# Kernel optimization log

Hardware: AMD Instinct MI355X
Metric: run time of the kernel (lower is better)

The kernel has to match this reference:

```python
import jax, jax.numpy as jnp
import numpy as np

N = 8192
E = 262144
H = 8
D_IN = 256
D_OUT = 256
D_PRIME = D_OUT // H  # is_concat=True


def setup_inputs() -> dict:
    key = jax.random.key(0)
    k_x, k_e, k_ww, k_wb, k_aw, k_ab = jax.random.split(key, 6)
    scale_w = 1.0 / np.sqrt(D_IN)
    scale_a = 1.0 / np.sqrt(2 * D_PRIME)
    return {
        "x": jax.random.normal(k_x, (N, D_IN), dtype=jnp.float32),
        "edge_index": jax.random.randint(k_e, (2, E), 0, N, dtype=jnp.int64),
        "W_w": jax.random.uniform(k_ww, (H, D_PRIME, D_IN), jnp.float32, -scale_w, scale_w),
        "W_b": jax.random.uniform(k_wb, (H, D_PRIME), jnp.float32, -scale_w, scale_w),
        "a_w": jax.random.uniform(k_aw, (H, 1, 2 * D_PRIME), jnp.float32, -scale_a, scale_a),
        "a_b": jax.random.uniform(k_ab, (H, 1), jnp.float32, -scale_a, scale_a),
    }


def reference(x, edge_index, W_w, W_b, a_w, a_b):
    n = x.shape[0]
    vi, vj = edge_index[0], edge_index[1]
    heads = []
    for k in range(W_w.shape[0]):  # small fixed head loop
        Wx = x @ W_w[k].T + W_b[k]                       # [N, d']
        pair = jnp.concatenate([Wx[vi], Wx[vj]], axis=-1)  # [E, 2d']
        e = jax.nn.leaky_relu(pair @ a_w[k].T + a_b[k], negative_slope=0.2)[:, 0]  # [E]
        # dense NxN score matrix: non-edges keep score 0 and DO participate in softmax,
        # duplicate edges accumulate -- matches torch scatter_add_ + Softmax(dim=-1)
        A = jnp.zeros((n, n), dtype=x.dtype).at[vi, vj].add(e)
        heads.append(jax.nn.softmax(A, axis=-1) @ Wx)     # [N, d']
    xp = jnp.stack(heads)                                 # [H, N, d']
    xp = jnp.transpose(xp, (1, 0, 2)).reshape(n, -1)      # is_concat=True
    return jax.nn.elu(xp)
```

## Files before the change

### kernel.cpp

```cpp
#include <hip/hip_runtime.h>


constexpr int N_NODES = 8192;
constexpr int E_EDGES = 262144;
constexpr int DIN = 256;
constexpr int DOUT = 256;
constexpr int MAXROW = 96;

__device__ __forceinline__ float leaky02(float v) { return v > 0.f ? v : 0.2f * v; }

__global__ __launch_bounds__(256) void gemm_fused(
    const float* __restrict__ x, const float* __restrict__ W,
    const float* __restrict__ Wb, const float* __restrict__ a_w,
    float* __restrict__ Wx, float* __restrict__ asrc_t,
    float* __restrict__ adst_t, float* __restrict__ colsum)
{
    __shared__ float As[16][68];
    __shared__ float Bs[16][68];
    __shared__ float redS[2][64];
    __shared__ float redD[2][64];
    __shared__ float csum[64];
    const int t = threadIdx.x;
    const int r0 = blockIdx.x * 64;
    const int c0 = blockIdx.y * 64;
    const int lr = t & 15, lc = t >> 4;
    const int sr = t >> 2, sk = (t & 3) * 4;

    if (t < 64) { redS[0][t] = 0.f; redS[1][t] = 0.f; redD[0][t] = 0.f; redD[1][t] = 0.f; csum[t] = 0.f; }

    float acc[4][4] = {};
    for (int kc = 0; kc < DIN; kc += 16) {
        float4 av = *(const float4*)&x[(size_t)(r0 + sr) * DIN + kc + sk];
        float4 bv = *(const float4*)&W[(size_t)(c0 + sr) * DIN + kc + sk];
        __syncthreads();
        As[sk + 0][sr] = av.x; As[sk + 1][sr] = av.y;
        As[sk + 2][sr] = av.z; As[sk + 3][sr] = av.w;
        Bs[sk + 0][sr] = bv.x; Bs[sk + 1][sr] = bv.y;
        Bs[sk + 2][sr] = bv.z; Bs[sk + 3][sr] = bv.w;
        __syncthreads();
#pragma unroll
        for (int k = 0; k < 16; ++k) {
            float4 a = *(const float4*)&As[k][lr * 4];
            float4 b = *(const float4*)&Bs[k][lc * 4];
            acc[0][0] += a.x * b.x; acc[0][1] += a.x * b.y; acc[0][2] += a.x * b.z; acc[0][3] += a.x * b.w;
            acc[1][0] += a.y * b.x; acc[1][1] += a.y * b.y; acc[1][2] += a.y * b.z; acc[1][3] += a.y * b.w;
            acc[2][0] += a.z * b.x; acc[2][1] += a.z * b.y; acc[2][2] += a.z * b.z; acc[2][3] += a.z * b.w;
            acc[3][0] += a.w * b.x; acc[3][1] += a.w * b.y; acc[3][2] += a.w * b.z; acc[3][3] += a.w * b.w;
        }
    }
    const int ccol = c0 + lc * 4;
    float4 bias = *(const float4*)&Wb[ccol];
#pragma unroll
    for (int i = 0; i < 4; ++i) {
        acc[i][0] += bias.x; acc[i][1] += bias.y; acc[i][2] += bias.z; acc[i][3] += bias.w;
        float4 o; o.x = acc[i][0]; o.y = acc[i][1]; o.z = acc[i][2]; o.w = acc[i][3];
        *(float4*)&Wx[(size_t)(r0 + lr * 4 + i) * DOUT + ccol] = o;
    }

    const int hloc = lc >> 3;
    const int hgl = blockIdx.y * 2 + hloc;
    const int dbase = (lc & 7) * 4;
    float aws[4], awd[4];
#pragma unroll
    for (int j = 0; j < 4; ++j) {
        aws[j] = a_w[hgl * 64 + dbase + j];
        awd[j] = a_w[hgl * 64 + 32 + dbase + j];
    }
#pragma unroll
    for (int i = 0; i < 4; ++i) {
        float ps = acc[i][0] * aws[0] + acc[i][1] * aws[1] + acc[i][2] * aws[2] + acc[i][3] * aws[3];
        float pd = acc[i][0] * awd[0] + acc[i][1] * awd[1] + acc[i][2] * awd[2] + acc[i][3] * awd[3];
        atomicAdd(&redS[hloc][lr * 4 + i], ps);
        atomicAdd(&redD[hloc][lr * 4 + i], pd);
    }
#pragma unroll
    for (int j = 0; j < 4; ++j)
        atomicAdd(&csum[lc * 4 + j], acc[0][j] + acc[1][j] + acc[2][j] + acc[3][j]);
    __syncthreads();
    if (t < 128) {
        int hh = t >> 6, r = t & 63;
        asrc_t[(size_t)(r0 + r) * 8 + blockIdx.y * 2 + hh] = redS[hh][r];
    } else {
        int u = t - 128; int hh = u >> 6, r = u & 63;
        adst_t[(size_t)(r0 + r) * 8 + blockIdx.y * 2 + hh] = redD[hh][r];
    }
    if (t < 64) atomicAdd(&colsum[c0 + t], csum[t]);
}

__global__ __launch_bounds__(256) void bucket_kernel(const int* __restrict__ eidx,
                                                     int* __restrict__ counts,
                                                     int* __restrict__ colbuf) {
    int e = blockIdx.x * 256 + threadIdx.x;
    int vi = eidx[e];
    int vj = eidx[E_EDGES + e];
    int c = atomicAdd(&counts[vi], 1);
    if (c < MAXROW) colbuf[(size_t)vi * MAXROW + c] = vj;
}

__global__ __launch_bounds__(256) void row_softmax(
    const int* __restrict__ counts, const int* __restrict__ colbuf,
    const float* __restrict__ Wx, const float* __restrict__ asrc_t,
    const float* __restrict__ adst_t, const float* __restrict__ a_b,
    const float* __restrict__ colsum, float* __restrict__ out)
{
    const int w = threadIdx.x >> 6;
    const int lane = threadIdx.x & 63;
    const int i = blockIdx.x * 4 + w;

    __shared__ alignas(16) int   colsL[4][MAXROW];
    __shared__ alignas(16) float wv[4][MAXROW][8];
    __shared__ alignas(16) float sv[4][MAXROW];

    int len = counts[i];
    if (len > MAXROW) len = MAXROW;

    for (int p = lane; p < len; p += 64) colsL[w][p] = colbuf[(size_t)i * MAXROW + p];
    __builtin_amdgcn_wave_barrier();

    const float4 as0 = *(const float4*)&asrc_t[(size_t)i * 8];
    const float4 as1 = *(const float4*)&asrc_t[(size_t)i * 8 + 4];
    const float4 ab0 = *(const float4*)&a_b[0];
    const float4 ab1 = *(const float4*)&a_b[4];
    float sab[8] = {as0.x + ab0.x, as0.y + ab0.y, as0.z + ab0.z, as0.w + ab0.w,
                    as1.x + ab1.x, as1.y + ab1.y, as1.z + ab1.z, as1.w + ab1.w};

    float base[8];

    if (len <= 64) {
        const bool act = lane < len;
        const int c = act ? colsL[w][lane] : 0;
        const int c_cmp = act ? c : (0x40000000 + lane);
        bool dupb = false;
        for (int k = 1; k < 64; ++k) {
            int cq = __shfl(c_cmp, (lane - k) & 63);
            dupb = dupb || ((k <= lane) && (cq == c_cmp));
        }
        const bool isrep = act && !dupb;
        const int nd = __popcll(__ballot(isrep));
        const bool anydup = (nd != len);

        const float4 ad0 = *(const float4*)&adst_t[(size_t)c * 8];
        const float4 ad1 = *(const float4*)&adst_t[(size_t)c * 8 + 4];
        float s[8], sm[8];
        s[0] = leaky02(sab[0] + ad0.x); s[1] = leaky02(sab[1] + ad0.y);
        s[2] = leaky02(sab[2] + ad0.z); s[3] = leaky02(sab[3] + ad0.w);
        s[4] = leaky02(sab[4] + ad1.x); s[5] = leaky02(sab[5] + ad1.y);
        s[6] = leaky02(sab[6] + ad1.z); s[7] = leaky02(sab[7] + ad1.w);
#pragma unroll
        for (int h = 0; h < 8; ++h) sm[h] = s[h];

        if (anydup) {
            for (int k = 1; k < 64; ++k) {
                const int sl = (lane + k) & 63;
                const int cq = __shfl(c_cmp, sl);
                const bool mz = (cq == c_cmp);
                float sq[8];
#pragma unroll
                for (int h = 0; h < 8; ++h) sq[h] = __shfl(s[h], sl);
                if (mz) {
#pragma unroll
                    for (int h = 0; h < 8; ++h) sm[h] += sq[h];
                }
            }
        }

        float val[8], enm[8], e[8];
#pragma unroll
        for (int h = 0; h < 8; ++h) val[h] = isrep ? sm[h] : 0.f;
#pragma unroll
        for (int st = 32; st; st >>= 1)
#pragma unroll
            for (int h = 0; h < 8; ++h) val[h] = fmaxf(val[h], __shfl_xor(val[h], st));
#pragma unroll
        for (int h = 0; h < 8; ++h) {
            float m = fmaxf(val[h], 0.f);
            enm[h] = __expf(-m);
            e[h] = isrep ? __expf(sm[h] - m) : 0.f;
            val[h] = e[h];
        }
#pragma unroll
        for (int st = 32; st; st >>= 1)
#pragma unroll
            for (int h = 0; h < 8; ++h) val[h] += __shfl_xor(val[h], st);
        float wt[8];
#pragma unroll
        for (int h = 0; h < 8; ++h) {
            float Z = val[h] + (float)(N_NODES - nd) * enm[h];
            float invZ = 1.f / Z;
            base[h] = enm[h] * invZ;
            wt[h] = isrep ? (e[h] - enm[h]) * invZ : 0.f;
        }
        if (act) {
            float4 w0; w0.x = wt[0]; w0.y = wt[1]; w0.z = wt[2]; w0.w = wt[3];
            float4 w1; w1.x = wt[4]; w1.y = wt[5]; w1.z = wt[6]; w1.w = wt[7];
            *(float4*)&wv[w][lane][0] = w0;
            *(float4*)&wv[w][lane][4] = w1;
        }
    } else {
        int repf0 = 0, repf1 = 0;
        {
            int p = lane;
            if (p < len) {
                int cc = colsL[w][p]; int r = 1;
                for (int q = 0; q < p; ++q) if (colsL[w][q] == cc) { r = 0; break; }
                repf0 = r;
            }
            p = lane + 64;
            if (p < len) {
                int cc = colsL[w][p]; int r = 1;
                for (int q = 0; q < p; ++q) if (colsL[w][q] == cc) { r = 0; break; }
                repf1 = r;
            }
        }
        int ndloc = repf0 + repf1;
#pragma unroll
        for (int st = 32; st; st >>= 1) ndloc += __shfl_xor(ndloc, st);
        const int nd = ndloc;
        for (int h = 0; h < 8; ++h) {
            for (int p = lane; p < len; p += 64)
                sv[w][p] = leaky02(sab[h] + adst_t[(size_t)colsL[w][p] * 8 + h]);
            __builtin_amdgcn_wave_barrier();
            float lmax = -1e30f, sm0 = 0.f, sm1 = 0.f;
            if (lane < len && repf0) {
                int cc = colsL[w][lane]; float a = sv[w][lane];
                for (int q = lane + 1; q < len; ++q) if (colsL[w][q] == cc) a += sv[w][q];
                sm0 = a; lmax = fmaxf(lmax, a);
            }
            if (lane + 64 < len && repf1) {
                int cc = colsL[w][lane + 64]; float a = sv[w][lane + 64];
                for (int q = lane + 65; q < len; ++q) if (colsL[w][q] == cc) a += sv[w][q];
                sm1 = a; lmax = fmaxf(lmax, a);
            }
#pragma unroll
            for (int st = 32; st; st >>= 1) lmax = fmaxf(lmax, __shfl_xor(lmax, st));
            const float mh = fmaxf(lmax, 0.f), enm = __expf(-mh);
            float e0 = (lane < len && repf0) ? __expf(sm0 - mh) : 0.f;
            float e1 = (lane + 64 < len && repf1) ? __expf(sm1 - mh) : 0.f;
            float lsum = e0 + e1;
#pragma unroll
            for (int st = 32; st; st >>= 1) lsum += __shfl_xor(lsum, st);
            const float Z = lsum + (float)(N_NODES - nd) * enm, invZ = 1.f / Z;
            base[h] = enm * invZ;
            if (lane < len)      wv[w][lane][h]      = repf0 ? (e0 - enm) * invZ : 0.f;
            if (lane + 64 < len) wv[w][lane + 64][h] = repf1 ? (e1 - enm) * invZ : 0.f;
            __builtin_amdgcn_wave_barrier();
        }
    }
    __builtin_amdgcn_wave_barrier();

    const int h4 = lane >> 3;
    float bsel = base[0];
#pragma unroll
    for (int h = 1; h < 8; ++h) bsel = (h4 == h) ? base[h] : bsel;

    float4 acc; acc.x = 0.f; acc.y = 0.f; acc.z = 0.f; acc.w = 0.f;
#pragma unroll 4
    for (int p = 0; p < len; ++p) {
        const int cp = colsL[w][p];
        const float wt = wv[w][p][h4];
        const float4 v = *(const float4*)&Wx[(size_t)cp * DOUT + lane * 4];
        acc.x = fmaf(wt, v.x, acc.x);
        acc.y = fmaf(wt, v.y, acc.y);
        acc.z = fmaf(wt, v.z, acc.z);
        acc.w = fmaf(wt, v.w, acc.w);
    }
    const float4 cs = *(const float4*)&colsum[lane * 4];
    float4 o;
    o.x = fmaf(bsel, cs.x, acc.x);
    o.y = fmaf(bsel, cs.y, acc.y);
    o.z = fmaf(bsel, cs.z, acc.z);
    o.w = fmaf(bsel, cs.w, acc.w);
    o.x = o.x > 0.f ? o.x : expm1f(o.x);
    o.y = o.y > 0.f ? o.y : expm1f(o.y);
    o.z = o.z > 0.f ? o.z : expm1f(o.z);
    o.w = o.w > 0.f ? o.w : expm1f(o.w);
    *(float4*)&out[(size_t)i * DOUT + lane * 4] = o;
}

extern "C" void kernel_launch(void* const* d_in, const int* in_sizes, int n_in,
                              void* d_out, int out_size, void* d_ws, size_t ws_size,
                              hipStream_t stream) {
    const float* x   = (const float*)d_in[0];
    const int*   ei  = (const int*)d_in[1];
    const float* W_w = (const float*)d_in[2];
    const float* W_b = (const float*)d_in[3];
    const float* a_w = (const float*)d_in[4];
    const float* a_b = (const float*)d_in[5];
    float* out = (float*)d_out;

    char* ws = (char*)d_ws;
    size_t off = 0;
    float* Wx = (float*)(ws + off);      off += (size_t)N_NODES * DOUT * 4;
    float* colsum = (float*)(ws + off);  size_t z0 = off; off += DOUT * 4;
    int* counts = (int*)(ws + off);      off += (size_t)N_NODES * 4;
    size_t zbytes = off - z0;
    int* colbuf = (int*)(ws + off);      off += (size_t)N_NODES * MAXROW * 4;
    float* asrc_t = (float*)(ws + off);  off += (size_t)N_NODES * 8 * 4;
    float* adst_t = (float*)(ws + off);  off += (size_t)N_NODES * 8 * 4;
    (void)ws_size; (void)in_sizes; (void)n_in; (void)out_size;

    hipMemsetAsync(ws + z0, 0, zbytes, stream);
    gemm_fused<<<dim3(N_NODES / 64, DOUT / 64), 256, 0, stream>>>(
        x, W_w, W_b, a_w, Wx, asrc_t, adst_t, colsum);
    bucket_kernel<<<E_EDGES / 256, 256, 0, stream>>>(ei, counts, colbuf);
    row_softmax<<<N_NODES / 4, 256, 0, stream>>>(counts, colbuf, Wx, asrc_t,
                                                 adst_t, a_b, colsum, out);
}
```

Before: 149.5 us.

## Fuse bucketing into GEMM launch, prefetch GEMM tiles, split softmax heads to cut registers

The edge-bucketing kernel is merged into the GEMM launch as extra blocks, each handling four edges per thread with vectorized index loads. This removes one kernel launch and lets bucketing run alongside the GEMM. The GEMM loop now loads the next k-tile from global memory before computing the current one, at the cost of a second barrier per iteration. The row softmax processes the 8 heads in two groups of 4 and keeps per-head base values in shared memory, which lowers register pressure and removes the per-lane select chain.

```diff
diff --git a/kernel.cpp b/kernel.cpp
--- a/kernel.cpp
+++ b/kernel.cpp
@@ -7,13 +7,18 @@
 constexpr int DOUT = 256;
 constexpr int MAXROW = 96;
 
+constexpr int GEMM_BLOCKS = (N_NODES / 64) * (DOUT / 64);
+constexpr int BUCKET_BLOCKS = E_EDGES / (256 * 4);
+
 __device__ __forceinline__ float leaky02(float v) { return v > 0.f ? v : 0.2f * v; }
 
-__global__ __launch_bounds__(256) void gemm_fused(
+__global__ __launch_bounds__(256) void gemm_bucket(
     const float* __restrict__ x, const float* __restrict__ W,
     const float* __restrict__ Wb, const float* __restrict__ a_w,
+    const int* __restrict__ eidx,
     float* __restrict__ Wx, float* __restrict__ asrc_t,
-    float* __restrict__ adst_t, float* __restrict__ colsum)
+    float* __restrict__ adst_t, float* __restrict__ colsum,
+    int* __restrict__ counts, int* __restrict__ colbuf)
 {
     __shared__ float As[16][68];
     __shared__ float Bs[16][68];
@@ -21,23 +26,41 @@
     __shared__ float redD[2][64];
     __shared__ float csum[64];
     const int t = threadIdx.x;
-    const int r0 = blockIdx.x * 64;
-    const int c0 = blockIdx.y * 64;
+
+    if (blockIdx.x >= GEMM_BLOCKS) {
+        const int e0 = (blockIdx.x - GEMM_BLOCKS) * 1024 + t * 4;
+        const int4 vi4 = *(const int4*)&eidx[e0];
+        const int4 vj4 = *(const int4*)&eidx[E_EDGES + e0];
+        int c;
+        c = atomicAdd(&counts[vi4.x], 1); if (c < MAXROW) colbuf[(size_t)vi4.x * MAXROW + c] = vj4.x;
+        c = atomicAdd(&counts[vi4.y], 1); if (c < MAXROW) colbuf[(size_t)vi4.y * MAXROW + c] = vj4.y;
+        c = atomicAdd(&counts[vi4.z], 1); if (c < MAXROW) colbuf[(size_t)vi4.z * MAXROW + c] = vj4.z;
+        c = atomicAdd(&counts[vi4.w], 1); if (c < MAXROW) colbuf[(size_t)vi4.w * MAXROW + c] = vj4.w;
+        return;
+    }
+
+    const int bx = blockIdx.x & 127;
+    const int by = blockIdx.x >> 7;
+    const int r0 = bx * 64;
+    const int c0 = by * 64;
     const int lr = t & 15, lc = t >> 4;
     const int sr = t >> 2, sk = (t & 3) * 4;
 
     if (t < 64) { redS[0][t] = 0.f; redS[1][t] = 0.f; redD[0][t] = 0.f; redD[1][t] = 0.f; csum[t] = 0.f; }
 
     float acc[4][4] = {};
-    for (int kc = 0; kc < DIN; kc += 16) {
-        float4 av = *(const float4*)&x[(size_t)(r0 + sr) * DIN + kc + sk];
-        float4 bv = *(const float4*)&W[(size_t)(c0 + sr) * DIN + kc + sk];
-        __syncthreads();
+    float4 av = *(const float4*)&x[(size_t)(r0 + sr) * DIN + sk];
+    float4 bv = *(const float4*)&W[(size_t)(c0 + sr) * DIN + sk];
+    for (int kc = 0; kc < 16; ++kc) {
         As[sk + 0][sr] = av.x; As[sk + 1][sr] = av.y;
         As[sk + 2][sr] = av.z; As[sk + 3][sr] = av.w;
         Bs[sk + 0][sr] = bv.x; Bs[sk + 1][sr] = bv.y;
         Bs[sk + 2][sr] = bv.z; Bs[sk + 3][sr] = bv.w;
         __syncthreads();
+        if (kc < 15) {
+            av = *(const float4*)&x[(size_t)(r0 + sr) * DIN + (kc + 1) * 16 + sk];
+            bv = *(const float4*)&W[(size_t)(c0 + sr) * DIN + (kc + 1) * 16 + sk];
+        }
 #pragma unroll
         for (int k = 0; k < 16; ++k) {
             float4 a = *(const float4*)&As[k][lr * 4];
@@ -47,6 +70,7 @@
             acc[2][0] += a.z * b.x; acc[2][1] += a.z * b.y; acc[2][2] += a.z * b.z; acc[2][3] += a.z * b.w;
             acc[3][0] += a.w * b.x; acc[3][1] += a.w * b.y; acc[3][2] += a.w * b.z; acc[3][3] += a.w * b.w;
         }
+        __syncthreads();
     }
     const int ccol = c0 + lc * 4;
     float4 bias = *(const float4*)&Wb[ccol];
@@ -58,7 +82,7 @@
     }
 
     const int hloc = lc >> 3;
-    const int hgl = blockIdx.y * 2 + hloc;
+    const int hgl = by * 2 + hloc;
     const int dbase = (lc & 7) * 4;
     float aws[4], awd[4];
 #pragma unroll
@@ -79,22 +103,12 @@
     __syncthreads();
     if (t < 128) {
         int hh = t >> 6, r = t & 63;
-        asrc_t[(size_t)(r0 + r) * 8 + blockIdx.y * 2 + hh] = redS[hh][r];
+        asrc_t[(size_t)(r0 + r) * 8 + by * 2 + hh] = redS[hh][r];
     } else {
         int u = t - 128; int hh = u >> 6, r = u & 63;
-        adst_t[(size_t)(r0 + r) * 8 + blockIdx.y * 2 + hh] = redD[hh][r];
+        adst_t[(size_t)(r0 + r) * 8 + by * 2 + hh] = redD[hh][r];
     }
     if (t < 64) atomicAdd(&colsum[c0 + t], csum[t]);
-}
-
-__global__ __launch_bounds__(256) void bucket_kernel(const int* __restrict__ eidx,
-                                                     int* __restrict__ counts,
-                                                     int* __restrict__ colbuf) {
-    int e = blockIdx.x * 256 + threadIdx.x;
-    int vi = eidx[e];
-    int vj = eidx[E_EDGES + e];
-    int c = atomicAdd(&counts[vi], 1);
-    if (c < MAXROW) colbuf[(size_t)vi * MAXROW + c] = vj;
 }
 
 __global__ __launch_bounds__(256) void row_softmax(
@@ -110,21 +124,13 @@
     __shared__ alignas(16) int   colsL[4][MAXROW];
     __shared__ alignas(16) float wv[4][MAXROW][8];
     __shared__ alignas(16) float sv[4][MAXROW];
+    __shared__ alignas(16) float base_s[4][8];
 
     int len = counts[i];
     if (len > MAXROW) len = MAXROW;
 
     for (int p = lane; p < len; p += 64) colsL[w][p] = colbuf[(size_t)i * MAXROW + p];
     __builtin_amdgcn_wave_barrier();
-
-    const float4 as0 = *(const float4*)&asrc_t[(size_t)i * 8];
-    const float4 as1 = *(const float4*)&asrc_t[(size_t)i * 8 + 4];
-    const float4 ab0 = *(const float4*)&a_b[0];
-    const float4 ab1 = *(const float4*)&a_b[4];
-    float sab[8] = {as0.x + ab0.x, as0.y + ab0.y, as0.z + ab0.z, as0.w + ab0.w,
-                    as1.x + ab1.x, as1.y + ab1.y, as1.z + ab1.z, as1.w + ab1.w};
-
-    float base[8];
 
     if (len <= 64) {
         const bool act = lane < len;
@@ -138,63 +144,69 @@
         const bool isrep = act && !dupb;
         const int nd = __popcll(__ballot(isrep));
         const bool anydup = (nd != len);
-
-        const float4 ad0 = *(const float4*)&adst_t[(size_t)c * 8];
-        const float4 ad1 = *(const float4*)&adst_t[(size_t)c * 8 + 4];
-        float s[8], sm[8];
-        s[0] = leaky02(sab[0] + ad0.x); s[1] = leaky02(sab[1] + ad0.y);
-        s[2] = leaky02(sab[2] + ad0.z); s[3] = leaky02(sab[3] + ad0.w);
-        s[4] = leaky02(sab[4] + ad1.x); s[5] = leaky02(sab[5] + ad1.y);
-        s[6] = leaky02(sab[6] + ad1.z); s[7] = leaky02(sab[7] + ad1.w);
-#pragma unroll
-        for (int h = 0; h < 8; ++h) sm[h] = s[h];
-
-        if (anydup) {
-            for (int k = 1; k < 64; ++k) {
-                const int sl = (lane + k) & 63;
-                const int cq = __shfl(c_cmp, sl);
-                const bool mz = (cq == c_cmp);
-                float sq[8];
-#pragma unroll
-                for (int h = 0; h < 8; ++h) sq[h] = __shfl(s[h], sl);
-                if (mz) {
-#pragma unroll
-                    for (int h = 0; h < 8; ++h) sm[h] += sq[h];
+        const float fnd = (float)(N_NODES - nd);
+
+#pragma unroll
+        for (int ck = 0; ck < 2; ++ck) {
+            const float4 as = *(const float4*)&asrc_t[(size_t)i * 8 + ck * 4];
+            const float4 ab = *(const float4*)&a_b[ck * 4];
+            const float4 ad = *(const float4*)&adst_t[(size_t)c * 8 + ck * 4];
+            float s[4], sm[4];
+            s[0] = leaky02(as.x + ab.x + ad.x);
+            s[1] = leaky02(as.y + ab.y + ad.y);
+            s[2] = leaky02(as.z + ab.z + ad.z);
+            s[3] = leaky02(as.w + ab.w + ad.w);
+#pragma unroll
+            for (int h = 0; h < 4; ++h) sm[h] = s[h];
+
+            if (anydup) {
+                for (int k = 1; k < 64; ++k) {
+                    const int sl = (lane + k) & 63;
+                    const int cq = __shfl(c_cmp, sl);
+                    float sq[4];
+#pragma unroll
+                    for (int h = 0; h < 4; ++h) sq[h] = __shfl(s[h], sl);
+                    if (cq == c_cmp) {
+#pragma unroll
+                        for (int h = 0; h < 4; ++h) sm[h] += sq[h];
+                    }
                 }
             }
-        }
-
-        float val[8], enm[8], e[8];
-#pragma unroll
-        for (int h = 0; h < 8; ++h) val[h] = isrep ? sm[h] : 0.f;
-#pragma unroll
-        for (int st = 32; st; st >>= 1)
-#pragma unroll
-            for (int h = 0; h < 8; ++h) val[h] = fmaxf(val[h], __shfl_xor(val[h], st));
-#pragma unroll
-        for (int h = 0; h < 8; ++h) {
-            float m = fmaxf(val[h], 0.f);
-            enm[h] = __expf(-m);
-            e[h] = isrep ? __expf(sm[h] - m) : 0.f;
-            val[h] = e[h];
-        }
-#pragma unroll
-        for (int st = 32; st; st >>= 1)
-#pragma unroll
-            for (int h = 0; h < 8; ++h) val[h] += __shfl_xor(val[h], st);
-        float wt[8];
-#pragma unroll
-        for (int h = 0; h < 8; ++h) {
-            float Z = val[h] + (float)(N_NODES - nd) * enm[h];
-            float invZ = 1.f / Z;
-            base[h] = enm[h] * invZ;
-            wt[h] = isrep ? (e[h] - enm[h]) * invZ : 0.f;
-        }
-        if (act) {
-            float4 w0; w0.x = wt[0]; w0.y = wt[1]; w0.z = wt[2]; w0.w = wt[3];
-            float4 w1; w1.x = wt[4]; w1.y = wt[5]; w1.z = wt[6]; w1.w = wt[7];
-            *(float4*)&wv[w][lane][0] = w0;
-            *(float4*)&wv[w][lane][4] = w1;
+
+            float val[4];
+#pragma unroll
+            for (int h = 0; h < 4; ++h) val[h] = isrep ? sm[h] : 0.f;
+#pragma unroll
+            for (int st = 32; st; st >>= 1)
+#pragma unroll
+                for (int h = 0; h < 4; ++h) val[h] = fmaxf(val[h], __shfl_xor(val[h], st));
+            float enm[4], e[4];
+#pragma unroll
+            for (int h = 0; h < 4; ++h) {
+                float m = fmaxf(val[h], 0.f);
+                enm[h] = __expf(-m);
+                e[h] = isrep ? __expf(sm[h] - m) : 0.f;
+                val[h] = e[h];
+            }
+#pragma unroll
+            for (int st = 32; st; st >>= 1)
+#pragma unroll
+                for (int h = 0; h < 4; ++h) val[h] += __shfl_xor(val[h], st);
+            float wt[4];
+#pragma unroll
+            for (int h = 0; h < 4; ++h) {
+                float invZ = 1.f / (val[h] + fnd * enm[h]);
+                wt[h] = isrep ? (e[h] - enm[h]) * invZ : 0.f;
+                enm[h] *= invZ;
+            }
+            if (act) {
+                float4 wq; wq.x = wt[0]; wq.y = wt[1]; wq.z = wt[2]; wq.w = wt[3];
+                *(float4*)&wv[w][lane][ck * 4] = wq;
+            }
+            if (lane == 0) {
+                float4 bq; bq.x = enm[0]; bq.y = enm[1]; bq.z = enm[2]; bq.w = enm[3];
+                *(float4*)&base_s[w][ck * 4] = bq;
+            }
         }
     } else {
         int repf0 = 0, repf1 = 0;
@@ -217,8 +229,9 @@
         for (int st = 32; st; st >>= 1) ndloc += __shfl_xor(ndloc, st);
         const int nd = ndloc;
         for (int h = 0; h < 8; ++h) {
+            const float sabh = asrc_t[(size_t)i * 8 + h] + a_b[h];
             for (int p = lane; p < len; p += 64)
-                sv[w][p] = leaky02(sab[h] + adst_t[(size_t)colsL[w][p] * 8 + h]);
+                sv[w][p] = leaky02(sabh + adst_t[(size_t)colsL[w][p] * 8 + h]);
             __builtin_amdgcn_wave_barrier();
             float lmax = -1e30f, sm0 = 0.f, sm1 = 0.f;
             if (lane < len && repf0) {
@@ -240,7 +253,7 @@
 #pragma unroll
             for (int st = 32; st; st >>= 1) lsum += __shfl_xor(lsum, st);
             const float Z = lsum + (float)(N_NODES - nd) * enm, invZ = 1.f / Z;
-            base[h] = enm * invZ;
+            if (lane == 0) base_s[w][h] = enm * invZ;
             if (lane < len)      wv[w][lane][h]      = repf0 ? (e0 - enm) * invZ : 0.f;
             if (lane + 64 < len) wv[w][lane + 64][h] = repf1 ? (e1 - enm) * invZ : 0.f;
             __builtin_amdgcn_wave_barrier();
@@ -249,9 +262,7 @@
     __builtin_amdgcn_wave_barrier();
 
     const int h4 = lane >> 3;
-    float bsel = base[0];
-#pragma unroll
-    for (int h = 1; h < 8; ++h) bsel = (h4 == h) ? base[h] : bsel;
+    const float bsel = base_s[w][h4];
 
     float4 acc; acc.x = 0.f; acc.y = 0.f; acc.z = 0.f; acc.w = 0.f;
 #pragma unroll 4
@@ -300,9 +311,8 @@
     (void)ws_size; (void)in_sizes; (void)n_in; (void)out_size;
 
     hipMemsetAsync(ws + z0, 0, zbytes, stream);
-    gemm_fused<<<dim3(N_NODES / 64, DOUT / 64), 256, 0, stream>>>(
-        x, W_w, W_b, a_w, Wx, asrc_t, adst_t, colsum);
-    bucket_kernel<<<E_EDGES / 256, 256, 0, stream>>>(ei, counts, colbuf);
+    gemm_bucket<<<GEMM_BLOCKS + BUCKET_BLOCKS, 256, 0, stream>>>(
+        x, W_w, W_b, a_w, ei, Wx, asrc_t, adst_t, colsum, counts, colbuf);
     row_softmax<<<N_NODES / 4, 256, 0, stream>>>(counts, colbuf, Wx, asrc_t,
                                                  adst_t, a_b, colsum, out);
 }
```

Result: faster. 144.4 us (-3.4%).
